# Optimization experiments

Hardware: AMD Instinct MI355X
Metric: run time of the kernel (lower is better)

## Reference

```python
import jax, jax.numpy as jnp
import numpy as np

N_HEADS = 16


def setup_inputs() -> dict:
    key = jax.random.key(0)
    ks = jax.random.split(key, 9)
    B, S, D = 2, 2048, 2048
    s = 0.02
    return {
        "X": jax.random.normal(ks[0], (B, S, D), jnp.float32),
        "Wq": jax.random.normal(ks[1], (D, D), jnp.float32) * s,
        "bq": jax.random.normal(ks[2], (D,), jnp.float32) * s,
        "Wk": jax.random.normal(ks[3], (D, D), jnp.float32) * s,
        "bk": jax.random.normal(ks[4], (D,), jnp.float32) * s,
        "Wv": jax.random.normal(ks[5], (D, D), jnp.float32) * s,
        "bv": jax.random.normal(ks[6], (D,), jnp.float32) * s,
        "Wo": jax.random.normal(ks[7], (D, D), jnp.float32) * s,
        "bo": jax.random.normal(ks[8], (D,), jnp.float32) * s,
    }


def reference(X, Wq, bq, Wk, bk, Wv, bv, Wo, bo):
    B, S, D = X.shape
    H = N_HEADS
    d_head = D // H
    # qk_scale = 1/sqrt(sqrt(d_head)), applied to BOTH Q and K
    scale = jnp.asarray(1.0 / np.sqrt(np.sqrt(d_head)), X.dtype)
    Q = (X @ Wq.T + bq).reshape(B, S, H, d_head) * scale  # bqhd
    K = (X @ Wk.T + bk).reshape(B, S, H, d_head) * scale  # bkhd
    V = (X @ Wv.T + bv).reshape(B, S, H, d_head)          # bkhd
    scores = jnp.einsum("bqhd,bkhd->bhqk", Q, K)
    causal = jnp.tril(jnp.ones((S, S), bool))  # [q, k]
    scores = jnp.where(causal[None, None], scores, -jnp.inf)
    # original casts logits to fp32 before softmax, back to Q dtype after
    attn = jax.nn.softmax(scores.astype(jnp.float32), axis=-1).astype(X.dtype)
    out = jnp.einsum("bhqk,bkhd->bqhd", attn, V).reshape(B, S, D)
    return out @ Wo.T + bo
```

## Files before the change

### kernel.cpp

```cpp
#include <hip/hip_runtime.h>


typedef __attribute__((ext_vector_type(8))) short bfx8;
typedef __attribute__((ext_vector_type(4))) float f32x4;

#define TO_GLOBAL(p) ((const __attribute__((address_space(1))) void*)(p))
#define TO_LDS(p)    ((__attribute__((address_space(3))) void*)(p))

__device__ __forceinline__ unsigned short f2bf(float f) {
    unsigned int u = __float_as_uint(f);
    u += 0x7FFFu + ((u >> 16) & 1u);
    return (unsigned short)(u >> 16);
}

__device__ __forceinline__ void store_out(unsigned short* p, float v) { *p = f2bf(v); }
__device__ __forceinline__ void store_out(float* p, float v) { *p = v; }

__global__ void cast_bf16_kernel(const float* __restrict__ x,
                                 unsigned short* __restrict__ y, int n4) {
    int i = blockIdx.x * blockDim.x + threadIdx.x;
    int st = gridDim.x * blockDim.x;
    for (; i < n4; i += st) {
        float4 v = reinterpret_cast<const float4*>(x)[i];
        ushort4 o;
        o.x = f2bf(v.x); o.y = f2bf(v.y); o.z = f2bf(v.z); o.w = f2bf(v.w);
        reinterpret_cast<ushort4*>(y)[i] = o;
    }
}

__global__ void cast3_kernel(const float* __restrict__ s0, const float* __restrict__ s1,
                             const float* __restrict__ s2,
                             unsigned short* __restrict__ d0, unsigned short* __restrict__ d1,
                             unsigned short* __restrict__ d2, int n4) {
    const float* s = (blockIdx.y == 0) ? s0 : (blockIdx.y == 1) ? s1 : s2;
    unsigned short* d = (blockIdx.y == 0) ? d0 : (blockIdx.y == 1) ? d1 : d2;
    int i = blockIdx.x * blockDim.x + threadIdx.x;
    int st = gridDim.x * blockDim.x;
    for (; i < n4; i += st) {
        float4 v = reinterpret_cast<const float4*>(s)[i];
        ushort4 o;
        o.x = f2bf(v.x); o.y = f2bf(v.y); o.z = f2bf(v.z); o.w = f2bf(v.w);
        reinterpret_cast<ushort4*>(d)[i] = o;
    }
}

template <typename OUT>
__global__ __launch_bounds__(256) void gemm_bt(
    const unsigned short* __restrict__ A, const unsigned short* __restrict__ Bw,
    const float* __restrict__ bias, OUT* __restrict__ C,
    int M, int N, int K, float scale) {
    __shared__ __align__(16) unsigned short Ash[128 * 32];
    __shared__ __align__(16) unsigned short Bsh[128 * 32];

    const int tid  = threadIdx.x;
    const int lane = tid & 63;
    const int w    = tid >> 6;
    const int g    = lane >> 4;
    const int l15  = lane & 15;
    const int m0   = blockIdx.y * 128;
    const int n0   = blockIdx.x * 128;
    const int wm   = (w >> 1) * 64;
    const int wn   = (w & 1) * 64;

    f32x4 acc[4][4];
#pragma unroll
    for (int i = 0; i < 4; i++)
#pragma unroll
        for (int j = 0; j < 4; j++) acc[i][j] = (f32x4){0.f, 0.f, 0.f, 0.f};

    const int c0 = tid, c1 = tid + 256;
    const int rowA0 = c0 >> 2, colA0 = (c0 & 3) * 8;
    const int rowA1 = c1 >> 2, colA1 = (c1 & 3) * 8;

    for (int k0 = 0; k0 < K; k0 += 32) {
        __syncthreads();
        __builtin_amdgcn_global_load_lds(TO_GLOBAL(A + (size_t)(m0 + rowA0) * K + k0 + colA0),
                                         TO_LDS(&Ash[c0 * 8]), 16, 0, 0);
        __builtin_amdgcn_global_load_lds(TO_GLOBAL(A + (size_t)(m0 + rowA1) * K + k0 + colA1),
                                         TO_LDS(&Ash[c1 * 8]), 16, 0, 0);
        __builtin_amdgcn_global_load_lds(TO_GLOBAL(Bw + (size_t)(n0 + rowA0) * K + k0 + colA0),
                                         TO_LDS(&Bsh[c0 * 8]), 16, 0, 0);
        __builtin_amdgcn_global_load_lds(TO_GLOBAL(Bw + (size_t)(n0 + rowA1) * K + k0 + colA1),
                                         TO_LDS(&Bsh[c1 * 8]), 16, 0, 0);
        __syncthreads();

        bfx8 af[4], bfr[4];
#pragma unroll
        for (int mi = 0; mi < 4; mi++)
            af[mi] = *reinterpret_cast<const bfx8*>(&Ash[(wm + mi * 16 + l15) * 32 + g * 8]);
#pragma unroll
        for (int ni = 0; ni < 4; ni++)
            bfr[ni] = *reinterpret_cast<const bfx8*>(&Bsh[(wn + ni * 16 + l15) * 32 + g * 8]);
#pragma unroll
        for (int mi = 0; mi < 4; mi++)
#pragma unroll
            for (int ni = 0; ni < 4; ni++)
                acc[mi][ni] = __builtin_amdgcn_mfma_f32_16x16x32_bf16(af[mi], bfr[ni],
                                                                     acc[mi][ni], 0, 0, 0);
    }

#pragma unroll
    for (int mi = 0; mi < 4; mi++) {
#pragma unroll
        for (int ni = 0; ni < 4; ni++) {
            const int col = n0 + wn + ni * 16 + l15;
            const float bv = bias[col];
#pragma unroll
            for (int r = 0; r < 4; r++) {
                const int row = m0 + wm + mi * 16 + g * 4 + r;
                store_out(&C[(size_t)row * N + col], (acc[mi][ni][r] + bv) * scale);
            }
        }
    }
}

__global__ __launch_bounds__(256) void gemm_qkv(
    const unsigned short* __restrict__ A,
    const unsigned short* __restrict__ W0, const unsigned short* __restrict__ W1,
    const unsigned short* __restrict__ W2,
    const float* __restrict__ b0, const float* __restrict__ b1,
    const float* __restrict__ b2,
    unsigned short* __restrict__ C0, unsigned short* __restrict__ C1,
    unsigned short* __restrict__ C2, float qks) {
    const int z = blockIdx.z;
    const unsigned short* Bw = (z == 0) ? W0 : (z == 1) ? W1 : W2;
    const float* bias = (z == 0) ? b0 : (z == 1) ? b1 : b2;
    unsigned short* C = (z == 0) ? C0 : (z == 1) ? C1 : C2;
    const float scale = (z < 2) ? qks : 1.0f;
    const int M = 4096, N = 2048, K = 2048;

    __shared__ __align__(16) unsigned short Ash[128 * 32];
    __shared__ __align__(16) unsigned short Bsh[128 * 32];

    const int tid  = threadIdx.x;
    const int lane = tid & 63;
    const int w    = tid >> 6;
    const int g    = lane >> 4;
    const int l15  = lane & 15;
    const int m0   = blockIdx.y * 128;
    const int n0   = blockIdx.x * 128;
    const int wm   = (w >> 1) * 64;
    const int wn   = (w & 1) * 64;

    f32x4 acc[4][4];
#pragma unroll
    for (int i = 0; i < 4; i++)
#pragma unroll
        for (int j = 0; j < 4; j++) acc[i][j] = (f32x4){0.f, 0.f, 0.f, 0.f};

    const int c0 = tid, c1 = tid + 256;
    const int rowA0 = c0 >> 2, colA0 = (c0 & 3) * 8;
    const int rowA1 = c1 >> 2, colA1 = (c1 & 3) * 8;

    for (int k0 = 0; k0 < K; k0 += 32) {
        __syncthreads();
        __builtin_amdgcn_global_load_lds(TO_GLOBAL(A + (size_t)(m0 + rowA0) * K + k0 + colA0),
                                         TO_LDS(&Ash[c0 * 8]), 16, 0, 0);
        __builtin_amdgcn_global_load_lds(TO_GLOBAL(A + (size_t)(m0 + rowA1) * K + k0 + colA1),
                                         TO_LDS(&Ash[c1 * 8]), 16, 0, 0);
        __builtin_amdgcn_global_load_lds(TO_GLOBAL(Bw + (size_t)(n0 + rowA0) * K + k0 + colA0),
                                         TO_LDS(&Bsh[c0 * 8]), 16, 0, 0);
        __builtin_amdgcn_global_load_lds(TO_GLOBAL(Bw + (size_t)(n0 + rowA1) * K + k0 + colA1),
                                         TO_LDS(&Bsh[c1 * 8]), 16, 0, 0);
        __syncthreads();

        bfx8 af[4], bfr[4];
#pragma unroll
        for (int mi = 0; mi < 4; mi++)
            af[mi] = *reinterpret_cast<const bfx8*>(&Ash[(wm + mi * 16 + l15) * 32 + g * 8]);
#pragma unroll
        for (int ni = 0; ni < 4; ni++)
            bfr[ni] = *reinterpret_cast<const bfx8*>(&Bsh[(wn + ni * 16 + l15) * 32 + g * 8]);
#pragma unroll
        for (int mi = 0; mi < 4; mi++)
#pragma unroll
            for (int ni = 0; ni < 4; ni++)
                acc[mi][ni] = __builtin_amdgcn_mfma_f32_16x16x32_bf16(af[mi], bfr[ni],
                                                                     acc[mi][ni], 0, 0, 0);
    }

#pragma unroll
    for (int mi = 0; mi < 4; mi++) {
#pragma unroll
        for (int ni = 0; ni < 4; ni++) {
            const int col = n0 + wn + ni * 16 + l15;
            const float bv = bias[col];
#pragma unroll
            for (int r = 0; r < 4; r++) {
                const int row = m0 + wm + mi * 16 + g * 4 + r;
                C[(size_t)row * N + col] = f2bf((acc[mi][ni][r] + bv) * scale);
            }
        }
    }
}

__global__ __launch_bounds__(256) void transpose_v(const unsigned short* __restrict__ V,
                                                   unsigned short* __restrict__ Vt) {
    __shared__ unsigned short tile[64][72];
    const int tid = threadIdx.x;
    const int r0 = blockIdx.y * 64;
    const int c0 = blockIdx.x * 64;
    const int b = r0 >> 11, sbase = r0 & 2047;
#pragma unroll
    for (int i = 0; i < 2; i++) {
        const int row = tid >> 2;
        const int ch  = (tid & 3) + 4 * i;
        bfx8 v = *reinterpret_cast<const bfx8*>(V + (size_t)(r0 + row) * 2048 + c0 + ch * 8);
        *reinterpret_cast<bfx8*>(&tile[row][ch * 8]) = v;
    }
    __syncthreads();
    const int dh  = tid & 63;
    const int s_l = (tid >> 6) * 16;
    unsigned short* dst = Vt + (size_t)(b * 2048 + c0 + dh) * 2048 + sbase + s_l;
#pragma unroll
    for (int half = 0; half < 2; half++) {
        bfx8 o;
#pragma unroll
        for (int j = 0; j < 8; j++) o[j] = (short)tile[s_l + half * 8 + j][dh];
        *reinterpret_cast<bfx8*>(dst + half * 8) = o;
    }
}

#define SLEN 2048
#define DMODEL 2048
#define M2FIX 11.541560327f

__global__ __launch_bounds__(256, 3) void attn_kernel(
    const unsigned short* __restrict__ Q, const unsigned short* __restrict__ Kp,
    const unsigned short* __restrict__ Vt, unsigned short* __restrict__ O) {
    __shared__ __align__(16) unsigned short Ksh[64 * 128];
    __shared__ __align__(16) unsigned short Vsh[128 * 64];
    __shared__ __align__(16) unsigned short Psh[4 * 1024];

    const int tid  = threadIdx.x;
    const int lane = tid & 63;
    const int w    = tid >> 6;
    const int g    = lane >> 4;
    const int l15  = lane & 15;
    const int bh   = blockIdx.x;
    const int b    = bh >> 4, h = bh & 15;
    const int pr   = blockIdx.y;

    const size_t bhbase = (size_t)b * SLEN * DMODEL + (size_t)h * 128;
    const size_t vtbase = (size_t)bh * 128 * SLEN;

    unsigned short* Pw = &Psh[w * 1024];
    const int khi_b = l15 >> 3, klo = l15 & 7;
    const int vsw = l15 & 7;

    const int krow = tid >> 4, kch = tid & 15;
    const int vdr  = tid >> 3, vch = tid & 7;

    bfx8 kreg[4], vreg[4];

#define LOADREGS(KB)                                                                \
    {                                                                               \
        _Pragma("unroll")                                                           \
        for (int i_ = 0; i_ < 4; i_++)                                              \
            kreg[i_] = *reinterpret_cast<const bfx8*>(                              \
                Kp + bhbase + (size_t)((KB) + krow + 16 * i_) * DMODEL + kch * 8);  \
        _Pragma("unroll")                                                           \
        for (int i_ = 0; i_ < 4; i_++)                                              \
            vreg[i_] = *reinterpret_cast<const bfx8*>(                              \
                Vt + vtbase + (size_t)(vdr + 32 * i_) * SLEN + (KB) + vch * 8);     \
    }

#pragma unroll 1
    for (int seg = 0; seg < 2; seg++) {
        const int qt  = seg == 0 ? (31 - pr) : pr;
        const int q0w = qt * 64 + w * 16;

        bfx8 qf[4];
#pragma unroll
        for (int c = 0; c < 4; c++)
            qf[c] = *reinterpret_cast<const bfx8*>(
                Q + bhbase + (size_t)(q0w + l15) * DMODEL + c * 32 + g * 8);

        f32x4 oacc[8];
#pragma unroll
        for (int i = 0; i < 8; i++) oacc[i] = (f32x4){0.f, 0.f, 0.f, 0.f};
        float lpart[4] = {0.f, 0.f, 0.f, 0.f};

        const int ntile = qt + 1;
        LOADREGS(0);

#pragma unroll 1
        for (int t = 0; t < ntile; t++) {
            const int kb = t * 64;
            __builtin_amdgcn_s_barrier();
            __builtin_amdgcn_sched_barrier(0);
#pragma unroll
            for (int i = 0; i < 4; i++) {
                const int row = krow + 16 * i;
                *reinterpret_cast<bfx8*>(&Ksh[row * 128 + ((kch ^ (row & 7)) * 8)]) = kreg[i];
            }
#pragma unroll
            for (int i = 0; i < 4; i++) {
                const int dr = vdr + 32 * i;
                *reinterpret_cast<bfx8*>(&Vsh[dr * 64 + ((vch ^ (dr & 7)) * 8)]) = vreg[i];
            }
            asm volatile("s_waitcnt lgkmcnt(0)" ::: "memory");
            __builtin_amdgcn_s_barrier();
            __builtin_amdgcn_sched_barrier(0);
            if (t + 1 < ntile) LOADREGS(kb + 64);

            __builtin_amdgcn_s_setprio(1);
            f32x4 sacc[4];
#pragma unroll
            for (int kt = 0; kt < 4; kt++) sacc[kt] = (f32x4){0.f, 0.f, 0.f, 0.f};
#pragma unroll
            for (int kt = 0; kt < 4; kt++) {
                const int row = kt * 16 + l15;
#pragma unroll
                for (int c = 0; c < 4; c++) {
                    bfx8 kf = *reinterpret_cast<const bfx8*>(
                        &Ksh[row * 128 + (((c * 4 + g) ^ (row & 7)) * 8)]);
                    sacc[kt] = __builtin_amdgcn_mfma_f32_16x16x32_bf16(
                        qf[c], kf, sacc[kt], 0, 0, 0);
                }
            }
            __builtin_amdgcn_s_setprio(0);
            if (t == ntile - 1) {
#pragma unroll
                for (int kt = 0; kt < 4; kt++)
#pragma unroll
                    for (int r = 0; r < 4; r++)
                        if (kb + kt * 16 + l15 > q0w + g * 4 + r)
                            sacc[kt][r] = -1e30f;
            }
#pragma unroll
            for (int r = 0; r < 4; r++) {
                const float p0 = exp2f(sacc[0][r] - M2FIX);
                const float p1 = exp2f(sacc[1][r] - M2FIX);
                const float p2 = exp2f(sacc[2][r] - M2FIX);
                const float p3 = exp2f(sacc[3][r] - M2FIX);
                lpart[r] += (p0 + p1) + (p2 + p3);
                const int ql = g * 4 + r;
                const int swz = ql & 7;
                Pw[ql * 64 + (((khi_b + 0) ^ swz) << 3) + klo] = f2bf(p0);
                Pw[ql * 64 + (((khi_b + 2) ^ swz) << 3) + klo] = f2bf(p1);
                Pw[ql * 64 + (((khi_b + 4) ^ swz) << 3) + klo] = f2bf(p2);
                Pw[ql * 64 + (((khi_b + 6) ^ swz) << 3) + klo] = f2bf(p3);
            }
            __builtin_amdgcn_s_setprio(1);
#pragma unroll
            for (int ks = 0; ks < 2; ks++) {
                bfx8 vb[8];
#pragma unroll
                for (int ni = 0; ni < 8; ni++) {
                    const int d = ni * 16 + l15;
                    vb[ni] = *reinterpret_cast<const bfx8*>(
                        &Vsh[d * 64 + (((ks * 4 + g) ^ vsw) * 8)]);
                }
                bfx8 pa = *reinterpret_cast<const bfx8*>(
                    Pw + l15 * 64 + (((ks * 4 + g) ^ vsw) << 3));
#pragma unroll
                for (int ni = 0; ni < 8; ni++)
                    oacc[ni] = __builtin_amdgcn_mfma_f32_16x16x32_bf16(
                        pa, vb[ni], oacc[ni], 0, 0, 0);
            }
            __builtin_amdgcn_s_setprio(0);
        }

#pragma unroll
        for (int r = 0; r < 4; r++) {
            float l = lpart[r];
#pragma unroll
            for (int s = 1; s < 16; s <<= 1) l += __shfl_xor(l, s);
            const float inv = 1.0f / l;
            const int q = q0w + g * 4 + r;
#pragma unroll
            for (int ni = 0; ni < 8; ni++)
                O[bhbase + (size_t)q * DMODEL + ni * 16 + l15] = f2bf(oacc[ni][r] * inv);
        }
    }
#undef LOADREGS
}

extern "C" void kernel_launch(void* const* d_in, const int* in_sizes, int n_in,
                              void* d_out, int out_size, void* d_ws, size_t ws_size,
                              hipStream_t stream) {
    const float* X  = (const float*)d_in[0];
    const float* Wq = (const float*)d_in[1];
    const float* bq = (const float*)d_in[2];
    const float* Wk = (const float*)d_in[3];
    const float* bk = (const float*)d_in[4];
    const float* Wv = (const float*)d_in[5];
    const float* bv = (const float*)d_in[6];
    const float* Wo = (const float*)d_in[7];
    const float* bo = (const float*)d_in[8];
    float* out = (float*)d_out;

    unsigned short* ws  = (unsigned short*)d_ws;
    unsigned short* Qb  = ws;
    unsigned short* Kb  = ws + 8388608;
    unsigned short* Vtb = ws + 16777216;
    unsigned short* XOb = ws + 25165824;
    unsigned short* Wb  = ws + 33554432;
    unsigned short* out_u   = (unsigned short*)d_out;
    unsigned short* Vstage  = out_u;
    unsigned short* Wkb     = out_u + 8388608;
    unsigned short* Wvb     = out_u + 12582912;

    const float qk_scale = 0.35709585f;

    const dim3 cb(256);

    cast_bf16_kernel<<<dim3(2048), cb, 0, stream>>>(X, XOb, 2097152);
    cast3_kernel<<<dim3(1024, 3), cb, 0, stream>>>(Wq, Wk, Wv, Wb, Wkb, Wvb, 1048576);

    gemm_qkv<<<dim3(16, 32, 3), cb, 0, stream>>>(XOb, Wb, Wkb, Wvb, bq, bk, bv,
                                                 Qb, Kb, Vstage, qk_scale);

    transpose_v<<<dim3(32, 64), cb, 0, stream>>>(Vstage, Vtb);

    attn_kernel<<<dim3(32, 16), cb, 0, stream>>>(Qb, Kb, Vtb, XOb);

    cast_bf16_kernel<<<dim3(1024), cb, 0, stream>>>(Wo, Wb, 1048576);
    gemm_bt<float><<<dim3(16, 32), cb, 0, stream>>>(XOb, Wb, bo, out, 4096, 2048, 2048, 1.0f);
}
```

Measured before the change: 282.5 us.

## Rewrite projection GEMMs as 8-wave 256x128 double-buffered pipelined kernels

Replaces both the QKV and output projection GEMMs with a shared core that uses 512 threads, 256x128 block tiles, a K-step of 64 and double-buffered LDS. Global-to-LDS prefetch of the next K-tile is interleaved with four MFMA quadrants, using explicit waitcnt, barriers and setprio. An XOR swizzle on the LDS layout is added to avoid bank conflicts. The intent is to hide memory latency and raise MFMA utilisation, at the cost of more LDS per block (96KB), hardcoded 2048 dimensions and fragile manual synchronisation.

```diff
diff --git a/kernel.cpp b/kernel.cpp
--- a/kernel.cpp
+++ b/kernel.cpp
@@ -45,22 +45,20 @@
 }
 
 template <typename OUT>
-__global__ __launch_bounds__(256) void gemm_bt(
+__device__ __forceinline__ void gemm8_core(
     const unsigned short* __restrict__ A, const unsigned short* __restrict__ Bw,
     const float* __restrict__ bias, OUT* __restrict__ C,
-    int M, int N, int K, float scale) {
-    __shared__ __align__(16) unsigned short Ash[128 * 32];
-    __shared__ __align__(16) unsigned short Bsh[128 * 32];
-
+    float scale, int m0, int n0,
+    unsigned short* Ash, unsigned short* Bsh) {
     const int tid  = threadIdx.x;
     const int lane = tid & 63;
     const int w    = tid >> 6;
     const int g    = lane >> 4;
     const int l15  = lane & 15;
-    const int m0   = blockIdx.y * 128;
-    const int n0   = blockIdx.x * 128;
-    const int wm   = (w >> 1) * 64;
-    const int wn   = (w & 1) * 64;
+    const int wm   = w >> 1;
+    const int wn   = w & 1;
+    const int srow = tid >> 3, sch = tid & 7;
+    const int swz  = l15 & 7;
 
     f32x4 acc[4][4];
 #pragma unroll
@@ -68,53 +66,145 @@
 #pragma unroll
         for (int j = 0; j < 4; j++) acc[i][j] = (f32x4){0.f, 0.f, 0.f, 0.f};
 
-    const int c0 = tid, c1 = tid + 256;
-    const int rowA0 = c0 >> 2, colA0 = (c0 & 3) * 8;
-    const int rowA1 = c1 >> 2, colA1 = (c1 & 3) * 8;
-
-    for (int k0 = 0; k0 < K; k0 += 32) {
-        __syncthreads();
-        __builtin_amdgcn_global_load_lds(TO_GLOBAL(A + (size_t)(m0 + rowA0) * K + k0 + colA0),
-                                         TO_LDS(&Ash[c0 * 8]), 16, 0, 0);
-        __builtin_amdgcn_global_load_lds(TO_GLOBAL(A + (size_t)(m0 + rowA1) * K + k0 + colA1),
-                                         TO_LDS(&Ash[c1 * 8]), 16, 0, 0);
-        __builtin_amdgcn_global_load_lds(TO_GLOBAL(Bw + (size_t)(n0 + rowA0) * K + k0 + colA0),
-                                         TO_LDS(&Bsh[c0 * 8]), 16, 0, 0);
-        __builtin_amdgcn_global_load_lds(TO_GLOBAL(Bw + (size_t)(n0 + rowA1) * K + k0 + colA1),
-                                         TO_LDS(&Bsh[c1 * 8]), 16, 0, 0);
-        __syncthreads();
-
-        bfx8 af[4], bfr[4];
-#pragma unroll
-        for (int mi = 0; mi < 4; mi++)
-            af[mi] = *reinterpret_cast<const bfx8*>(&Ash[(wm + mi * 16 + l15) * 32 + g * 8]);
-#pragma unroll
-        for (int ni = 0; ni < 4; ni++)
-            bfr[ni] = *reinterpret_cast<const bfx8*>(&Bsh[(wn + ni * 16 + l15) * 32 + g * 8]);
-#pragma unroll
-        for (int mi = 0; mi < 4; mi++)
-#pragma unroll
-            for (int ni = 0; ni < 4; ni++)
-                acc[mi][ni] = __builtin_amdgcn_mfma_f32_16x16x32_bf16(af[mi], bfr[ni],
-                                                                     acc[mi][ni], 0, 0, 0);
+#define STGA(BUF, Q_, KB)                                                            \
+    __builtin_amdgcn_global_load_lds(                                                \
+        TO_GLOBAL(A + (size_t)(m0 + (Q_) * 64 + srow) * 2048 + (KB) +                \
+                  ((sch ^ (srow & 7)) * 8)),                                         \
+        TO_LDS(Ash + (BUF) * 16384 + (Q_) * 4096 + tid * 8), 16, 0, 0)
+#define STGB(BUF, H_, KB)                                                            \
+    __builtin_amdgcn_global_load_lds(                                                \
+        TO_GLOBAL(Bw + (size_t)(n0 + (H_) * 64 + srow) * 2048 + (KB) +               \
+                  ((sch ^ (srow & 7)) * 8)),                                         \
+        TO_LDS(Bsh + (BUF) * 8192 + (H_) * 4096 + tid * 8), 16, 0, 0)
+
+    STGA(0, 0, 0); STGA(0, 1, 0); STGA(0, 2, 0); STGA(0, 3, 0);
+    STGB(0, 0, 0); STGB(0, 1, 0);
+
+#pragma unroll 1
+    for (int t = 0; t < 32; ++t) {
+        const int kb = t * 64;
+        const int cb = t & 1, nb = cb ^ 1;
+        const bool pf = (t + 1 < 32);
+        if (pf) {
+            STGA(nb, 0, kb + 64);
+            asm volatile("s_waitcnt vmcnt(1)" ::: "memory");
+        } else {
+            asm volatile("s_waitcnt vmcnt(0)" ::: "memory");
+        }
+        __builtin_amdgcn_s_barrier();
+
+        const unsigned short* Ab = Ash + cb * 16384;
+        const unsigned short* Bb = Bsh + cb * 8192;
+        bfx8 a0[2][2], a1[2][2], b0[2][2], b1[2][2];
+
+#pragma unroll
+        for (int mi = 0; mi < 2; mi++)
+#pragma unroll
+            for (int kc = 0; kc < 2; kc++)
+                a0[mi][kc] = *(const bfx8*)(Ab + (wm * 64 + mi * 16 + l15) * 64 +
+                                            (((kc * 4 + g) ^ swz) * 8));
+#pragma unroll
+        for (int ni = 0; ni < 2; ni++)
+#pragma unroll
+            for (int kc = 0; kc < 2; kc++)
+                b0[ni][kc] = *(const bfx8*)(Bb + (wn * 64 + ni * 16 + l15) * 64 +
+                                            (((kc * 4 + g) ^ swz) * 8));
+        if (pf) STGA(nb, 1, kb + 64);
+        __builtin_amdgcn_s_barrier();
+        asm volatile("s_waitcnt lgkmcnt(0)" ::: "memory");
+        __builtin_amdgcn_sched_barrier(0);
+        __builtin_amdgcn_s_setprio(1);
+#pragma unroll
+        for (int kc = 0; kc < 2; kc++)
+#pragma unroll
+            for (int mi = 0; mi < 2; mi++)
+#pragma unroll
+                for (int ni = 0; ni < 2; ni++)
+                    acc[mi][ni] = __builtin_amdgcn_mfma_f32_16x16x32_bf16(
+                        a0[mi][kc], b0[ni][kc], acc[mi][ni], 0, 0, 0);
+        __builtin_amdgcn_s_setprio(0);
+        __builtin_amdgcn_s_barrier();
+
+#pragma unroll
+        for (int ni = 0; ni < 2; ni++)
+#pragma unroll
+            for (int kc = 0; kc < 2; kc++)
+                b1[ni][kc] = *(const bfx8*)(Bb + (wn * 64 + 32 + ni * 16 + l15) * 64 +
+                                            (((kc * 4 + g) ^ swz) * 8));
+        if (pf) STGA(nb, 2, kb + 64);
+        __builtin_amdgcn_s_barrier();
+        asm volatile("s_waitcnt lgkmcnt(0)" ::: "memory");
+        __builtin_amdgcn_sched_barrier(0);
+        __builtin_amdgcn_s_setprio(1);
+#pragma unroll
+        for (int kc = 0; kc < 2; kc++)
+#pragma unroll
+            for (int mi = 0; mi < 2; mi++)
+#pragma unroll
+                for (int ni = 0; ni < 2; ni++)
+                    acc[mi][ni + 2] = __builtin_amdgcn_mfma_f32_16x16x32_bf16(
+                        a0[mi][kc], b1[ni][kc], acc[mi][ni + 2], 0, 0, 0);
+        __builtin_amdgcn_s_setprio(0);
+        __builtin_amdgcn_s_barrier();
+
+#pragma unroll
+        for (int mi = 0; mi < 2; mi++)
+#pragma unroll
+            for (int kc = 0; kc < 2; kc++)
+                a1[mi][kc] = *(const bfx8*)(Ab + (wm * 64 + 32 + mi * 16 + l15) * 64 +
+                                            (((kc * 4 + g) ^ swz) * 8));
+        if (pf) STGA(nb, 3, kb + 64);
+        __builtin_amdgcn_s_barrier();
+        asm volatile("s_waitcnt lgkmcnt(0)" ::: "memory");
+        __builtin_amdgcn_sched_barrier(0);
+        __builtin_amdgcn_s_setprio(1);
+#pragma unroll
+        for (int kc = 0; kc < 2; kc++)
+#pragma unroll
+            for (int mi = 0; mi < 2; mi++)
+#pragma unroll
+                for (int ni = 0; ni < 2; ni++)
+                    acc[mi + 2][ni + 2] = __builtin_amdgcn_mfma_f32_16x16x32_bf16(
+                        a1[mi][kc], b1[ni][kc], acc[mi + 2][ni + 2], 0, 0, 0);
+        __builtin_amdgcn_s_setprio(0);
+        __builtin_amdgcn_s_barrier();
+
+        if (pf) { STGB(nb, 0, kb + 64); STGB(nb, 1, kb + 64); }
+        __builtin_amdgcn_s_barrier();
+        __builtin_amdgcn_s_setprio(1);
+#pragma unroll
+        for (int kc = 0; kc < 2; kc++)
+#pragma unroll
+            for (int mi = 0; mi < 2; mi++)
+#pragma unroll
+                for (int ni = 0; ni < 2; ni++)
+                    acc[mi + 2][ni] = __builtin_amdgcn_mfma_f32_16x16x32_bf16(
+                        a1[mi][kc], b0[ni][kc], acc[mi + 2][ni], 0, 0, 0);
+        __builtin_amdgcn_s_setprio(0);
+        __builtin_amdgcn_s_barrier();
     }
 
 #pragma unroll
     for (int mi = 0; mi < 4; mi++) {
+        const int rbase = m0 + wm * 64 + (mi >> 1) * 32 + (mi & 1) * 16;
 #pragma unroll
         for (int ni = 0; ni < 4; ni++) {
-            const int col = n0 + wn + ni * 16 + l15;
+            const int col = n0 + wn * 64 + (ni >> 1) * 32 + (ni & 1) * 16 + l15;
             const float bv = bias[col];
 #pragma unroll
             for (int r = 0; r < 4; r++) {
-                const int row = m0 + wm + mi * 16 + g * 4 + r;
-                store_out(&C[(size_t)row * N + col], (acc[mi][ni][r] + bv) * scale);
+                const int row = rbase + g * 4 + r;
+                store_out(&C[(size_t)row * 2048 + col], (acc[(mi & 1) + (mi >> 1) * 2]
+                          [(ni & 1) + (ni >> 1) * 2][r] + bv) * scale);
             }
         }
     }
-}
-
-__global__ __launch_bounds__(256) void gemm_qkv(
+#undef STGA
+#undef STGB
+}
+
+
+__global__ __launch_bounds__(512, 2) void gemm8_qkv(
     const unsigned short* __restrict__ A,
     const unsigned short* __restrict__ W0, const unsigned short* __restrict__ W1,
     const unsigned short* __restrict__ W2,
@@ -122,76 +212,24 @@
     const float* __restrict__ b2,
     unsigned short* __restrict__ C0, unsigned short* __restrict__ C1,
     unsigned short* __restrict__ C2, float qks) {
+    __shared__ __align__(16) unsigned short Ash[2 * 16384];
+    __shared__ __align__(16) unsigned short Bsh[2 * 8192];
     const int z = blockIdx.z;
     const unsigned short* Bw = (z == 0) ? W0 : (z == 1) ? W1 : W2;
     const float* bias = (z == 0) ? b0 : (z == 1) ? b1 : b2;
     unsigned short* C = (z == 0) ? C0 : (z == 1) ? C1 : C2;
     const float scale = (z < 2) ? qks : 1.0f;
-    const int M = 4096, N = 2048, K = 2048;
-
-    __shared__ __align__(16) unsigned short Ash[128 * 32];
-    __shared__ __align__(16) unsigned short Bsh[128 * 32];
-
-    const int tid  = threadIdx.x;
-    const int lane = tid & 63;
-    const int w    = tid >> 6;
-    const int g    = lane >> 4;
-    const int l15  = lane & 15;
-    const int m0   = blockIdx.y * 128;
-    const int n0   = blockIdx.x * 128;
-    const int wm   = (w >> 1) * 64;
-    const int wn   = (w & 1) * 64;
-
-    f32x4 acc[4][4];
-#pragma unroll
-    for (int i = 0; i < 4; i++)
-#pragma unroll
-        for (int j = 0; j < 4; j++) acc[i][j] = (f32x4){0.f, 0.f, 0.f, 0.f};
-
-    const int c0 = tid, c1 = tid + 256;
-    const int rowA0 = c0 >> 2, colA0 = (c0 & 3) * 8;
-    const int rowA1 = c1 >> 2, colA1 = (c1 & 3) * 8;
-
-    for (int k0 = 0; k0 < K; k0 += 32) {
-        __syncthreads();
-        __builtin_amdgcn_global_load_lds(TO_GLOBAL(A + (size_t)(m0 + rowA0) * K + k0 + colA0),
-                                         TO_LDS(&Ash[c0 * 8]), 16, 0, 0);
-        __builtin_amdgcn_global_load_lds(TO_GLOBAL(A + (size_t)(m0 + rowA1) * K + k0 + colA1),
-                                         TO_LDS(&Ash[c1 * 8]), 16, 0, 0);
-        __builtin_amdgcn_global_load_lds(TO_GLOBAL(Bw + (size_t)(n0 + rowA0) * K + k0 + colA0),
-                                         TO_LDS(&Bsh[c0 * 8]), 16, 0, 0);
-        __builtin_amdgcn_global_load_lds(TO_GLOBAL(Bw + (size_t)(n0 + rowA1) * K + k0 + colA1),
-                                         TO_LDS(&Bsh[c1 * 8]), 16, 0, 0);
-        __syncthreads();
-
-        bfx8 af[4], bfr[4];
-#pragma unroll
-        for (int mi = 0; mi < 4; mi++)
-            af[mi] = *reinterpret_cast<const bfx8*>(&Ash[(wm + mi * 16 + l15) * 32 + g * 8]);
-#pragma unroll
-        for (int ni = 0; ni < 4; ni++)
-            bfr[ni] = *reinterpret_cast<const bfx8*>(&Bsh[(wn + ni * 16 + l15) * 32 + g * 8]);
-#pragma unroll
-        for (int mi = 0; mi < 4; mi++)
-#pragma unroll
-            for (int ni = 0; ni < 4; ni++)
-                acc[mi][ni] = __builtin_amdgcn_mfma_f32_16x16x32_bf16(af[mi], bfr[ni],
-                                                                     acc[mi][ni], 0, 0, 0);
-    }
-
-#pragma unroll
-    for (int mi = 0; mi < 4; mi++) {
-#pragma unroll
-        for (int ni = 0; ni < 4; ni++) {
-            const int col = n0 + wn + ni * 16 + l15;
-            const float bv = bias[col];
-#pragma unroll
-            for (int r = 0; r < 4; r++) {
-                const int row = m0 + wm + mi * 16 + g * 4 + r;
-                C[(size_t)row * N + col] = f2bf((acc[mi][ni][r] + bv) * scale);
-            }
-        }
-    }
+    gemm8_core<unsigned short>(A, Bw, bias, C, scale,
+                               blockIdx.y * 256, blockIdx.x * 128, Ash, Bsh);
+}
+
+__global__ __launch_bounds__(512, 2) void gemm8_out(
+    const unsigned short* __restrict__ A, const unsigned short* __restrict__ Bw,
+    const float* __restrict__ bias, float* __restrict__ C) {
+    __shared__ __align__(16) unsigned short Ash[2 * 16384];
+    __shared__ __align__(16) unsigned short Bsh[2 * 8192];
+    gemm8_core<float>(A, Bw, bias, C, 1.0f,
+                      blockIdx.y * 256, blockIdx.x * 128, Ash, Bsh);
 }
 
 __global__ __launch_bounds__(256) void transpose_v(const unsigned short* __restrict__ V,
@@ -409,13 +447,13 @@
     cast_bf16_kernel<<<dim3(2048), cb, 0, stream>>>(X, XOb, 2097152);
     cast3_kernel<<<dim3(1024, 3), cb, 0, stream>>>(Wq, Wk, Wv, Wb, Wkb, Wvb, 1048576);
 
-    gemm_qkv<<<dim3(16, 32, 3), cb, 0, stream>>>(XOb, Wb, Wkb, Wvb, bq, bk, bv,
-                                                 Qb, Kb, Vstage, qk_scale);
+    gemm8_qkv<<<dim3(16, 16, 3), dim3(512), 0, stream>>>(XOb, Wb, Wkb, Wvb, bq, bk, bv,
+                                                         Qb, Kb, Vstage, qk_scale);
 
     transpose_v<<<dim3(32, 64), cb, 0, stream>>>(Vstage, Vtb);
 
     attn_kernel<<<dim3(32, 16), cb, 0, stream>>>(Qb, Kb, Vtb, XOb);
 
     cast_bf16_kernel<<<dim3(1024), cb, 0, stream>>>(Wo, Wb, 1048576);
-    gemm_bt<float><<<dim3(16, 32), cb, 0, stream>>>(XOb, Wb, bo, out, 4096, 2048, 2048, 1.0f);
-}
+    gemm8_out<<<dim3(16, 16), dim3(512), 0, stream>>>(XOb, Wb, bo, out);
+}
```

After: 308.5 us. 1.09x slower.

## Rewrite QKV GEMM as 256x256 double-buffered, swizzled, phased MFMA pipeline

Applied to the files above, without the earlier changes.

Replaces the 128x128 single-buffered QKV projection GEMM with a 512-thread 256x256 tile kernel. It uses double-buffered LDS with an XOR-swizzled layout and K-steps of 64. Global-to-LDS prefetch of the next stage is interleaved across four MFMA phases, each gated by barriers and priority hints. The goal is to hide global load latency, cut LDS bank conflicts and raise arithmetic intensity per tile. In exchange it uses 128KB of LDS and many more accumulator registers, which limits occupancy.

```diff
diff --git a/kernel.cpp b/kernel.cpp
--- a/kernel.cpp
+++ b/kernel.cpp
@@ -114,84 +114,164 @@
     }
 }
 
-__global__ __launch_bounds__(256) void gemm_qkv(
+__global__ __launch_bounds__(512, 2) void gemm256_qkv(
     const unsigned short* __restrict__ A,
     const unsigned short* __restrict__ W0, const unsigned short* __restrict__ W1,
     const unsigned short* __restrict__ W2,
-    const float* __restrict__ b0, const float* __restrict__ b1,
-    const float* __restrict__ b2,
+    const float* __restrict__ b0p, const float* __restrict__ b1p,
+    const float* __restrict__ b2p,
     unsigned short* __restrict__ C0, unsigned short* __restrict__ C1,
     unsigned short* __restrict__ C2, float qks) {
+    __shared__ __align__(16) unsigned short Ash[32768];
+    __shared__ __align__(16) unsigned short Bsh[32768];
+
     const int z = blockIdx.z;
     const unsigned short* Bw = (z == 0) ? W0 : (z == 1) ? W1 : W2;
-    const float* bias = (z == 0) ? b0 : (z == 1) ? b1 : b2;
+    const float* bias = (z == 0) ? b0p : (z == 1) ? b1p : b2p;
     unsigned short* C = (z == 0) ? C0 : (z == 1) ? C1 : C2;
     const float scale = (z < 2) ? qks : 1.0f;
-    const int M = 4096, N = 2048, K = 2048;
-
-    __shared__ __align__(16) unsigned short Ash[128 * 32];
-    __shared__ __align__(16) unsigned short Bsh[128 * 32];
 
     const int tid  = threadIdx.x;
     const int lane = tid & 63;
     const int w    = tid >> 6;
     const int g    = lane >> 4;
     const int l15  = lane & 15;
-    const int m0   = blockIdx.y * 128;
-    const int n0   = blockIdx.x * 128;
-    const int wm   = (w >> 1) * 64;
-    const int wn   = (w & 1) * 64;
-
-    f32x4 acc[4][4];
-#pragma unroll
-    for (int i = 0; i < 4; i++)
+    const int wm   = w >> 2;
+    const int wn   = w & 3;
+    const int m0   = blockIdx.y * 256;
+    const int n0   = blockIdx.x * 256;
+    const int sch  = tid & 7;
+
+    f32x4 acc[8][4];
+#pragma unroll
+    for (int i = 0; i < 8; i++)
 #pragma unroll
         for (int j = 0; j < 4; j++) acc[i][j] = (f32x4){0.f, 0.f, 0.f, 0.f};
 
-    const int c0 = tid, c1 = tid + 256;
-    const int rowA0 = c0 >> 2, colA0 = (c0 & 3) * 8;
-    const int rowA1 = c1 >> 2, colA1 = (c1 & 3) * 8;
-
-    for (int k0 = 0; k0 < K; k0 += 32) {
-        __syncthreads();
-        __builtin_amdgcn_global_load_lds(TO_GLOBAL(A + (size_t)(m0 + rowA0) * K + k0 + colA0),
-                                         TO_LDS(&Ash[c0 * 8]), 16, 0, 0);
-        __builtin_amdgcn_global_load_lds(TO_GLOBAL(A + (size_t)(m0 + rowA1) * K + k0 + colA1),
-                                         TO_LDS(&Ash[c1 * 8]), 16, 0, 0);
-        __builtin_amdgcn_global_load_lds(TO_GLOBAL(Bw + (size_t)(n0 + rowA0) * K + k0 + colA0),
-                                         TO_LDS(&Bsh[c0 * 8]), 16, 0, 0);
-        __builtin_amdgcn_global_load_lds(TO_GLOBAL(Bw + (size_t)(n0 + rowA1) * K + k0 + colA1),
-                                         TO_LDS(&Bsh[c1 * 8]), 16, 0, 0);
-        __syncthreads();
-
-        bfx8 af[4], bfr[4];
-#pragma unroll
-        for (int mi = 0; mi < 4; mi++)
-            af[mi] = *reinterpret_cast<const bfx8*>(&Ash[(wm + mi * 16 + l15) * 32 + g * 8]);
-#pragma unroll
-        for (int ni = 0; ni < 4; ni++)
-            bfr[ni] = *reinterpret_cast<const bfx8*>(&Bsh[(wn + ni * 16 + l15) * 32 + g * 8]);
-#pragma unroll
-        for (int mi = 0; mi < 4; mi++)
-#pragma unroll
-            for (int ni = 0; ni < 4; ni++)
-                acc[mi][ni] = __builtin_amdgcn_mfma_f32_16x16x32_bf16(af[mi], bfr[ni],
-                                                                     acc[mi][ni], 0, 0, 0);
-    }
-
-#pragma unroll
-    for (int mi = 0; mi < 4; mi++) {
-#pragma unroll
-        for (int ni = 0; ni < 4; ni++) {
-            const int col = n0 + wn + ni * 16 + l15;
+#define STG_A(BUF, H, KB)                                                            \
+    do {                                                                             \
+        _Pragma("unroll")                                                            \
+        for (int L_ = 0; L_ < 2; ++L_) {                                             \
+            const int r_ = L_ * 64 + (tid >> 3);                                     \
+            __builtin_amdgcn_global_load_lds(                                        \
+                TO_GLOBAL(A + (size_t)(m0 + (H) * 128 + r_) * 2048 + (KB) +          \
+                          ((sch ^ (r_ & 7)) * 8)),                                   \
+                TO_LDS(Ash + (BUF) * 16384 + (H) * 8192 + L_ * 4096 + tid * 8),      \
+                16, 0, 0);                                                           \
+        }                                                                            \
+    } while (0)
+#define STG_B(BUF, H, KB)                                                            \
+    do {                                                                             \
+        _Pragma("unroll")                                                            \
+        for (int L_ = 0; L_ < 2; ++L_) {                                             \
+            const int r_ = L_ * 64 + (tid >> 3);                                     \
+            __builtin_amdgcn_global_load_lds(                                        \
+                TO_GLOBAL(Bw + (size_t)(n0 + (H) * 128 + r_) * 2048 + (KB) +         \
+                          ((sch ^ (r_ & 7)) * 8)),                                   \
+                TO_LDS(Bsh + (BUF) * 16384 + (H) * 8192 + L_ * 4096 + tid * 8),      \
+                16, 0, 0);                                                           \
+        }                                                                            \
+    } while (0)
+
+#define RD_A(DST, BUF, MH)                                                           \
+    _Pragma("unroll")                                                                \
+    for (int mi = 0; mi < 4; mi++)                                                   \
+        _Pragma("unroll")                                                            \
+        for (int kc = 0; kc < 2; kc++) {                                             \
+            const int r_ = (MH) * 64 + mi * 16 + l15;                                \
+            DST[mi][kc] = *(const bfx8*)(Ash + (BUF) * 16384 + wm * 8192 +           \
+                                         r_ * 64 + (((kc * 4 + g) ^ (r_ & 7)) * 8)); \
+        }
+#define RD_B(DST, BUF, NH)                                                           \
+    _Pragma("unroll")                                                                \
+    for (int ni = 0; ni < 2; ni++)                                                   \
+        _Pragma("unroll")                                                            \
+        for (int kc = 0; kc < 2; kc++) {                                             \
+            const int r_ = (wn & 1) * 64 + (NH) * 32 + ni * 16 + l15;                \
+            DST[ni][kc] = *(const bfx8*)(Bsh + (BUF) * 16384 + (wn >> 1) * 8192 +    \
+                                         r_ * 64 + (((kc * 4 + g) ^ (r_ & 7)) * 8)); \
+        }
+#define MFMA16(AF, BF, MH, NH)                                                       \
+    __builtin_amdgcn_s_setprio(1);                                                   \
+    _Pragma("unroll")                                                                \
+    for (int kc = 0; kc < 2; kc++)                                                   \
+        _Pragma("unroll")                                                            \
+        for (int mi = 0; mi < 4; mi++)                                               \
+            _Pragma("unroll")                                                        \
+            for (int ni = 0; ni < 2; ni++)                                           \
+                acc[(MH) * 4 + mi][(NH) * 2 + ni] =                                  \
+                    __builtin_amdgcn_mfma_f32_16x16x32_bf16(                         \
+                        AF[mi][kc], BF[ni][kc], acc[(MH) * 4 + mi][(NH) * 2 + ni],   \
+                        0, 0, 0);                                                    \
+    __builtin_amdgcn_s_setprio(0);
+
+    STG_A(0, 0, 0); STG_A(0, 1, 0); STG_B(0, 0, 0); STG_B(0, 1, 0);
+
+    bfx8 a0[4][2], a1[4][2], bb[2][2];
+
+#pragma unroll 1
+    for (int t = 0; t < 32; ++t) {
+        const int kb  = t * 64;
+        const int buf = t & 1;
+        const bool pf = (t + 1 < 32);
+
+        if (pf) {
+            STG_A(buf ^ 1, 0, kb + 64);
+            asm volatile("s_waitcnt vmcnt(2)" ::: "memory");
+        } else {
+            asm volatile("s_waitcnt vmcnt(0)" ::: "memory");
+        }
+        RD_A(a0, buf, 0);
+        RD_B(bb, buf, 0);
+        __builtin_amdgcn_s_barrier();
+        asm volatile("s_waitcnt lgkmcnt(0)" ::: "memory");
+        __builtin_amdgcn_sched_barrier(0);
+        MFMA16(a0, bb, 0, 0);
+        __builtin_amdgcn_s_barrier();
+
+        if (pf) STG_A(buf ^ 1, 1, kb + 64);
+        RD_B(bb, buf, 1);
+        __builtin_amdgcn_s_barrier();
+        asm volatile("s_waitcnt lgkmcnt(0)" ::: "memory");
+        __builtin_amdgcn_sched_barrier(0);
+        MFMA16(a0, bb, 0, 1);
+        __builtin_amdgcn_s_barrier();
+
+        if (pf) STG_B(buf ^ 1, 0, kb + 64);
+        RD_A(a1, buf, 1);
+        __builtin_amdgcn_s_barrier();
+        asm volatile("s_waitcnt lgkmcnt(0)" ::: "memory");
+        __builtin_amdgcn_sched_barrier(0);
+        MFMA16(a1, bb, 1, 1);
+        __builtin_amdgcn_s_barrier();
+
+        if (pf) STG_B(buf ^ 1, 1, kb + 64);
+        RD_B(bb, buf, 0);
+        __builtin_amdgcn_s_barrier();
+        asm volatile("s_waitcnt lgkmcnt(0)" ::: "memory");
+        __builtin_amdgcn_sched_barrier(0);
+        MFMA16(a1, bb, 1, 0);
+        __builtin_amdgcn_s_barrier();
+    }
+
+#pragma unroll
+    for (int mf = 0; mf < 8; mf++) {
+#pragma unroll
+        for (int nf = 0; nf < 4; nf++) {
+            const int col = n0 + wn * 64 + nf * 16 + l15;
             const float bv = bias[col];
 #pragma unroll
             for (int r = 0; r < 4; r++) {
-                const int row = m0 + wm + mi * 16 + g * 4 + r;
-                C[(size_t)row * N + col] = f2bf((acc[mi][ni][r] + bv) * scale);
-            }
-        }
-    }
+                const int row = m0 + wm * 128 + mf * 16 + g * 4 + r;
+                C[(size_t)row * 2048 + col] = f2bf((acc[mf][nf][r] + bv) * scale);
+            }
+        }
+    }
+#undef STG_A
+#undef STG_B
+#undef RD_A
+#undef RD_B
+#undef MFMA16
 }
 
 __global__ __launch_bounds__(256) void transpose_v(const unsigned short* __restrict__ V,
@@ -409,8 +489,8 @@
     cast_bf16_kernel<<<dim3(2048), cb, 0, stream>>>(X, XOb, 2097152);
     cast3_kernel<<<dim3(1024, 3), cb, 0, stream>>>(Wq, Wk, Wv, Wb, Wkb, Wvb, 1048576);
 
-    gemm_qkv<<<dim3(16, 32, 3), cb, 0, stream>>>(XOb, Wb, Wkb, Wvb, bq, bk, bv,
-                                                 Qb, Kb, Vstage, qk_scale);
+    gemm256_qkv<<<dim3(8, 16, 3), dim3(512), 0, stream>>>(XOb, Wb, Wkb, Wvb, bq, bk, bv,
+                                                          Qb, Kb, Vstage, qk_scale);
 
     transpose_v<<<dim3(32, 64), cb, 0, stream>>>(Vstage, Vtb);
 
```

New measurement: 347.0 us. 22.8% more time.

## Fuse V transpose into QKV GEMM epilogue and swizzle GEMM blocks across XCDs

Applied to the files above, without the earlier changes.

The QKV GEMM now writes V straight into the transposed [b, d, s] layout in its epilogue, using 4-element vector stores along the sequence dimension, so the separate transpose_v kernel and its staging buffer are removed. Both GEMM kernels also remap block indices so that consecutive blocks dispatched to the same XCD cover neighbouring tiles, which should improve L2 reuse. The transposed V stores are strided across rows and may coalesce worse than row-major stores, and the output-buffer staging offsets were rearranged to match.

```diff
diff --git a/kernel.cpp b/kernel.cpp
--- a/kernel.cpp
+++ b/kernel.cpp
@@ -44,6 +44,13 @@
     }
 }
 
+__device__ __forceinline__ void xcd_swizzle_16x32(int& bx, int& by) {
+    const int lin = by * 16 + bx;
+    const int wl  = (lin & 7) * 64 + (lin >> 3);
+    bx = wl & 15;
+    by = wl >> 4;
+}
+
 template <typename OUT>
 __global__ __launch_bounds__(256) void gemm_bt(
     const unsigned short* __restrict__ A, const unsigned short* __restrict__ Bw,
@@ -57,8 +64,10 @@
     const int w    = tid >> 6;
     const int g    = lane >> 4;
     const int l15  = lane & 15;
-    const int m0   = blockIdx.y * 128;
-    const int n0   = blockIdx.x * 128;
+    int bx = blockIdx.x, by = blockIdx.y;
+    xcd_swizzle_16x32(bx, by);
+    const int m0   = by * 128;
+    const int n0   = bx * 128;
     const int wm   = (w >> 1) * 64;
     const int wn   = (w & 1) * 64;
 
@@ -127,7 +136,7 @@
     const float* bias = (z == 0) ? b0 : (z == 1) ? b1 : b2;
     unsigned short* C = (z == 0) ? C0 : (z == 1) ? C1 : C2;
     const float scale = (z < 2) ? qks : 1.0f;
-    const int M = 4096, N = 2048, K = 2048;
+    const int N = 2048, K = 2048;
 
     __shared__ __align__(16) unsigned short Ash[128 * 32];
     __shared__ __align__(16) unsigned short Bsh[128 * 32];
@@ -137,8 +146,10 @@
     const int w    = tid >> 6;
     const int g    = lane >> 4;
     const int l15  = lane & 15;
-    const int m0   = blockIdx.y * 128;
-    const int n0   = blockIdx.x * 128;
+    int bx = blockIdx.x, by = blockIdx.y;
+    xcd_swizzle_16x32(bx, by);
+    const int m0   = by * 128;
+    const int n0   = bx * 128;
     const int wm   = (w >> 1) * 64;
     const int wn   = (w & 1) * 64;
 
@@ -179,45 +190,38 @@
                                                                      acc[mi][ni], 0, 0, 0);
     }
 
-#pragma unroll
-    for (int mi = 0; mi < 4; mi++) {
-#pragma unroll
-        for (int ni = 0; ni < 4; ni++) {
-            const int col = n0 + wn + ni * 16 + l15;
-            const float bv = bias[col];
-#pragma unroll
-            for (int r = 0; r < 4; r++) {
-                const int row = m0 + wm + mi * 16 + g * 4 + r;
-                C[(size_t)row * N + col] = f2bf((acc[mi][ni][r] + bv) * scale);
+    if (z == 2) {
+#pragma unroll
+        for (int mi = 0; mi < 4; mi++) {
+            const int rbase = m0 + wm + mi * 16 + g * 4;
+            const int b_ = rbase >> 11;
+            const int sbase = rbase & 2047;
+#pragma unroll
+            for (int ni = 0; ni < 4; ni++) {
+                const int col = n0 + wn + ni * 16 + l15;
+                const float bv = bias[col];
+                ushort4 o;
+                o.x = f2bf(acc[mi][ni][0] + bv);
+                o.y = f2bf(acc[mi][ni][1] + bv);
+                o.z = f2bf(acc[mi][ni][2] + bv);
+                o.w = f2bf(acc[mi][ni][3] + bv);
+                *reinterpret_cast<ushort4*>(C + ((size_t)(b_ * 2048 + col)) * 2048 + sbase) = o;
             }
         }
-    }
-}
-
-__global__ __launch_bounds__(256) void transpose_v(const unsigned short* __restrict__ V,
-                                                   unsigned short* __restrict__ Vt) {
-    __shared__ unsigned short tile[64][72];
-    const int tid = threadIdx.x;
-    const int r0 = blockIdx.y * 64;
-    const int c0 = blockIdx.x * 64;
-    const int b = r0 >> 11, sbase = r0 & 2047;
-#pragma unroll
-    for (int i = 0; i < 2; i++) {
-        const int row = tid >> 2;
-        const int ch  = (tid & 3) + 4 * i;
-        bfx8 v = *reinterpret_cast<const bfx8*>(V + (size_t)(r0 + row) * 2048 + c0 + ch * 8);
-        *reinterpret_cast<bfx8*>(&tile[row][ch * 8]) = v;
-    }
-    __syncthreads();
-    const int dh  = tid & 63;
-    const int s_l = (tid >> 6) * 16;
-    unsigned short* dst = Vt + (size_t)(b * 2048 + c0 + dh) * 2048 + sbase + s_l;
-#pragma unroll
-    for (int half = 0; half < 2; half++) {
-        bfx8 o;
-#pragma unroll
-        for (int j = 0; j < 8; j++) o[j] = (short)tile[s_l + half * 8 + j][dh];
-        *reinterpret_cast<bfx8*>(dst + half * 8) = o;
+    } else {
+#pragma unroll
+        for (int mi = 0; mi < 4; mi++) {
+#pragma unroll
+            for (int ni = 0; ni < 4; ni++) {
+                const int col = n0 + wn + ni * 16 + l15;
+                const float bv = bias[col];
+#pragma unroll
+                for (int r = 0; r < 4; r++) {
+                    const int row = m0 + wm + mi * 16 + g * 4 + r;
+                    C[(size_t)row * N + col] = f2bf((acc[mi][ni][r] + bv) * scale);
+                }
+            }
+        }
     }
 }
 
@@ -397,10 +401,9 @@
     unsigned short* Vtb = ws + 16777216;
     unsigned short* XOb = ws + 25165824;
     unsigned short* Wb  = ws + 33554432;
-    unsigned short* out_u   = (unsigned short*)d_out;
-    unsigned short* Vstage  = out_u;
-    unsigned short* Wkb     = out_u + 8388608;
-    unsigned short* Wvb     = out_u + 12582912;
+    unsigned short* out_u = (unsigned short*)d_out;
+    unsigned short* Wkb   = out_u;
+    unsigned short* Wvb   = out_u + 4194304;
 
     const float qk_scale = 0.35709585f;
 
@@ -410,9 +413,7 @@
     cast3_kernel<<<dim3(1024, 3), cb, 0, stream>>>(Wq, Wk, Wv, Wb, Wkb, Wvb, 1048576);
 
     gemm_qkv<<<dim3(16, 32, 3), cb, 0, stream>>>(XOb, Wb, Wkb, Wvb, bq, bk, bv,
-                                                 Qb, Kb, Vstage, qk_scale);
-
-    transpose_v<<<dim3(32, 64), cb, 0, stream>>>(Vstage, Vtb);
+                                                 Qb, Kb, Vtb, qk_scale);
 
     attn_kernel<<<dim3(32, 16), cb, 0, stream>>>(Qb, Kb, Vtb, XOb);
 
```

After: 288.3 us. +2.1%, slower.
